# Performance work log

Measured on AMD Instinct MI355X. Metric: run time of the kernel, lower is better.

The kernel has to match this reference:

```python
import jax, jax.numpy as jnp
import numpy as np

N = 100000
E = 1600000
EMB = 64
IN = 64
HID = 64
HEADS = 3
NEG_SLOPE = 0.2            # PyG GATConv default LeakyReLU slope
RRELU_SLOPE = (1.0 / 8.0 + 1.0 / 3.0) / 2.0  # torch.rrelu eval-mode slope


def setup_inputs() -> dict:
    key = jax.random.key(0)
    ks = jax.random.split(key, 16)
    d_in = IN + EMB
    inp = {
        "z": jax.random.normal(ks[0], (N, EMB), jnp.float32),
        "x": jax.random.normal(ks[1], (N, IN), jnp.float32),
        "edge_index": jax.random.randint(ks[2], (2, E), 0, N, jnp.int32),
        # gat1: (in+emb) -> hidden, 3 heads, concat=False
        "W1": jax.random.normal(ks[3], (d_in, HEADS * HID), jnp.float32) / np.sqrt(d_in),
        "att_src1": jax.random.normal(ks[4], (HEADS, HID), jnp.float32) / np.sqrt(HID),
        "att_dst1": jax.random.normal(ks[5], (HEADS, HID), jnp.float32) / np.sqrt(HID),
        "bias1": jnp.zeros((HID,), jnp.float32),
        # gat2: hidden -> hidden, 3 heads, concat=True
        "W2": jax.random.normal(ks[6], (HID, HEADS * HID), jnp.float32) / np.sqrt(HID),
        "att_src2": jax.random.normal(ks[7], (HEADS, HID), jnp.float32) / np.sqrt(HID),
        "att_dst2": jax.random.normal(ks[8], (HEADS, HID), jnp.float32) / np.sqrt(HID),
        "bias2": jnp.zeros((HEADS * HID,), jnp.float32),
        # final linear hidden*3 -> 1 (with bias)
        "lin_w": jax.random.normal(ks[9], (HEADS * HID, 1), jnp.float32) / np.sqrt(HEADS * HID),
        "lin_b": jnp.zeros((1,), jnp.float32),
    }
    return inp


def rrelu_eval(x):
    return jnp.where(x >= 0, x, x * RRELU_SLOPE)


def gat_conv(x, src, dst, W, a_src, a_dst, bias, concat):
    """PyG GATConv (shared src/dst projection, self-loops already appended)."""
    n = x.shape[0]
    H, C = a_src.shape
    xl = (x @ W).reshape(n, H, C)                       # [N, H, C]
    s = jnp.einsum('nhc,hc->nh', xl, a_src)             # alpha_src per node
    d = jnp.einsum('nhc,hc->nh', xl, a_dst)             # alpha_dst per node
    alpha = jax.nn.leaky_relu(s[src] + d[dst], NEG_SLOPE)  # [E', H]
    amax = jax.ops.segment_max(alpha, dst, num_segments=n)
    ex = jnp.exp(alpha - amax[dst])
    denom = jax.ops.segment_sum(ex, dst, num_segments=n)
    w = ex / (denom[dst] + 1e-16)                       # segment softmax
    out = jax.ops.segment_sum(xl[src] * w[:, :, None], dst, num_segments=n)  # [N,H,C]
    out = out.reshape(n, H * C) if concat else out.mean(axis=1)
    return out + bias


def reference(z, x, edge_index, W1, att_src1, att_dst1, bias1,
              W2, att_src2, att_dst2, bias2, lin_w, lin_b):
    n = x.shape[0]
    loops = jnp.arange(n, dtype=edge_index.dtype)
    src = jnp.concatenate([edge_index[0], loops])       # add self-loops (PyG default)
    dst = jnp.concatenate([edge_index[1], loops])
    h = jnp.concatenate([z, x], axis=1)
    h = rrelu_eval(gat_conv(h, src, dst, W1, att_src1, att_dst1, bias1, concat=False))
    h = rrelu_eval(gat_conv(h, src, dst, W2, att_src2, att_dst2, bias2, concat=True))
    return h @ lin_w + lin_b
```

## Files before the change

kernel.cpp:

```cpp
#include <hip/hip_runtime.h>
#include <cstdint>
#include <cstddef>

#define NEG_SLOPE 0.2f
#define RRELU_SLOPE 0.22916666666666666f

#define BSHIFT 6
#define BCAP 1536
#define MAXNB 1600

typedef _Float16 half4 __attribute__((ext_vector_type(4)));
typedef _Float16 half8 __attribute__((ext_vector_type(8)));
typedef float f32x4 __attribute__((ext_vector_type(4)));

__device__ __forceinline__ float wave_sum64(float v) {
#pragma unroll
  for (int o = 32; o > 0; o >>= 1) v += __shfl_xor(v, o, 64);
  return v;
}

__global__ __launch_bounds__(256) void wcvt_kernel(const float* __restrict__ W1,
                                                   const float* __restrict__ W2,
                                                   _Float16* __restrict__ Wt1,
                                                   _Float16* __restrict__ Wt2) {
  const int c = blockIdx.x;
  for (int k = threadIdx.x; k < 128; k += 256)
    Wt1[(size_t)c * 128 + k] = (_Float16)W1[(size_t)k * 192 + c];
  for (int k = threadIdx.x; k < 64; k += 256)
    Wt2[(size_t)c * 64 + k] = (_Float16)W2[(size_t)k * 192 + c];
}

__device__ __forceinline__ void bucketA_body(char* smem, int bid, int nblk,
                                             const int* __restrict__ src,
                                             const int* __restrict__ dst, int E, int NB,
                                             int* __restrict__ cursor,
                                             int* __restrict__ region) {
  int* hist = (int*)smem;
  int* gbase = hist + MAXNB;
  const int tid = threadIdx.x;
  const int chunk = (E + nblk - 1) / nblk;
  const int e0 = bid * chunk;
  const int e1 = min(e0 + chunk, E);
  for (int b = tid; b < NB; b += 256) hist[b] = 0;
  __syncthreads();
  for (int i = e0 + tid; i < e1; i += 256) {
    atomicAdd(&hist[dst[i] >> BSHIFT], 1);
  }
  __syncthreads();
  for (int b = tid; b < NB; b += 256) {
    int c = hist[b];
    gbase[b] = (c > 0) ? atomicAdd(&cursor[b], c) : 0;
    hist[b] = 0;
  }
  __syncthreads();
  for (int i = e0 + tid; i < e1; i += 256) {
    int d = dst[i];
    int b = d >> BSHIFT;
    int idx = atomicAdd(&hist[b], 1) + gbase[b];
    if (idx < BCAP) region[b * BCAP + idx] = src[i] | ((d & 63) << 17);
  }
}

__global__ __launch_bounds__(256) void bucket_scan(const int* __restrict__ cursor, int NB,
                                                   int* __restrict__ colbase) {
  __shared__ int lds[256];
  const int tid = threadIdx.x;
  const int K = (NB + 255) / 256;
  int vals[8];
  int s = 0;
#pragma unroll
  for (int j = 0; j < 8; j++) {
    int b = tid * K + j;
    int v = (j < K && b < NB) ? (min(cursor[b], BCAP) + 64) : 0;
    vals[j] = v;
    s += v;
  }
  lds[tid] = s;
  __syncthreads();
  for (int o = 1; o < 256; o <<= 1) {
    int t = (tid >= o) ? lds[tid - o] : 0;
    __syncthreads();
    lds[tid] += t;
    __syncthreads();
  }
  int off = (tid > 0) ? lds[tid - 1] : 0;
#pragma unroll
  for (int j = 0; j < 8; j++) {
    int b = tid * K + j;
    if (j < K && b < NB) colbase[b] = off;
    off += vals[j];
  }
}

__global__ __launch_bounds__(256) void bucketB(const int* __restrict__ region,
                                               const int* __restrict__ cursor,
                                               const int* __restrict__ colbase, int NB,
                                               int* __restrict__ rp, int* __restrict__ col) {
  __shared__ int lcnt[64];
  __shared__ int loff[64];
  const int b = blockIdx.x;
  const int tid = threadIdx.x;
  const int cnt = min(cursor[b], BCAP);
  const int base = colbase[b];
  if (tid < 64) lcnt[tid] = 0;
  __syncthreads();
  const int* reg = region + (size_t)b * BCAP;
  for (int i = tid; i < cnt; i += 256) {
    atomicAdd(&lcnt[reg[i] >> 17], 1);
  }
  __syncthreads();
  if (tid < 64) {
    int v = lcnt[tid] + 1;
    int inc = v;
#pragma unroll
    for (int o = 1; o < 64; o <<= 1) {
      int t = __shfl_up(inc, o, 64);
      if (tid >= o) inc += t;
    }
    int excl = inc - v;
    loff[tid] = excl;
    int n = (b << BSHIFT) + tid;
    rp[n] = base + excl;
    col[base + excl] = n;
    lcnt[tid] = 1;
  }
  __syncthreads();
  for (int i = tid; i < cnt; i += 256) {
    int r = reg[i];
    int ld = r >> 17;
    int idx = atomicAdd(&lcnt[ld], 1);
    col[base + loff[ld] + idx] = r & 0x1FFFF;
  }
}

#define APAD 72
#define BTPAD 72
#define GEMM_LDS (64 * APAD * 2 + 192 * BTPAD * 2)

template <int KC>
__device__ __forceinline__ void gemm_body(char* smem, int bid,
    const float* __restrict__ A0, const float* __restrict__ A1,
    const _Float16* __restrict__ Wt, const float* __restrict__ asrc,
    const float* __restrict__ adst, _Float16* __restrict__ xlh,
    float* __restrict__ sdS, float* __restrict__ sdD, int N) {
  _Float16* A16 = (_Float16*)smem;
  _Float16* Bt = A16 + 64 * APAD;
  const int tid = threadIdx.x;
  const int w = tid >> 6;
  const int lane = tid & 63;
  const int m = lane & 15;
  const int q = lane >> 4;
  const int m0 = bid * 64;
  const int KW = KC * 64;

  f32x4 acc[12];
#pragma unroll
  for (int t = 0; t < 12; t++) acc[t] = (f32x4)(0.f);

  for (int kc = 0; kc < KC; kc++) {
    const float* __restrict__ Ab = (KC == 2 && kc == 1) ? A1 : A0;
    if (kc > 0) __syncthreads();
#pragma unroll
    for (int i = 0; i < 4; i++) {
      int f = tid + 256 * i;
      int row = f >> 4;
      int c4 = f & 15;
      int gr = m0 + row;
      gr = (gr < N) ? gr : (N - 1);
      float4 v = *(const float4*)(Ab + (size_t)gr * 64 + c4 * 4);
      half4 hv;
      hv.x = (_Float16)v.x; hv.y = (_Float16)v.y;
      hv.z = (_Float16)v.z; hv.w = (_Float16)v.w;
      *(half4*)&A16[row * APAD + c4 * 4] = hv;
    }
#pragma unroll
    for (int i = 0; i < 6; i++) {
      int f = tid + 256 * i;
      int kg = f / 192;
      int c = f % 192;
      half8 hv = *(const half8*)&Wt[(size_t)c * KW + kc * 64 + kg * 8];
      *(half8*)&Bt[c * BTPAD + kg * 8] = hv;
    }
    __syncthreads();

#pragma unroll
    for (int t = 0; t < 2; t++) {
      half8 af = *(const half8*)&A16[(w * 16 + m) * APAD + t * 32 + q * 8];
#pragma unroll
      for (int ct = 0; ct < 12; ct++) {
        half8 bf = *(const half8*)&Bt[(ct * 16 + m) * BTPAD + t * 32 + q * 8];
        acc[ct] = __builtin_amdgcn_mfma_f32_16x16x32_f16(af, bf, acc[ct], 0, 0, 0);
      }
    }
  }

  float avs[12], avd[12];
#pragma unroll
  for (int ct = 0; ct < 12; ct++) {
    avs[ct] = asrc[ct * 16 + m];
    avd[ct] = adst[ct * 16 + m];
  }
#pragma unroll
  for (int r = 0; r < 4; r++) {
    const int gr = m0 + w * 16 + q * 4 + r;
    const bool ok = gr < N;
    if (ok) {
#pragma unroll
      for (int ct = 0; ct < 12; ct++) {
        xlh[(size_t)gr * 192 + ct * 16 + m] = (_Float16)acc[ct][r];
      }
    }
#pragma unroll
    for (int h = 0; h < 3; h++) {
      float ps = acc[h * 4 + 0][r] * avs[h * 4 + 0] + acc[h * 4 + 1][r] * avs[h * 4 + 1] +
                 acc[h * 4 + 2][r] * avs[h * 4 + 2] + acc[h * 4 + 3][r] * avs[h * 4 + 3];
      float pd = acc[h * 4 + 0][r] * avd[h * 4 + 0] + acc[h * 4 + 1][r] * avd[h * 4 + 1] +
                 acc[h * 4 + 2][r] * avd[h * 4 + 2] + acc[h * 4 + 3][r] * avd[h * 4 + 3];
#pragma unroll
      for (int o = 1; o < 16; o <<= 1) {
        ps += __shfl_xor(ps, o, 64);
        pd += __shfl_xor(pd, o, 64);
      }
      if (ok && m == 0) {
        sdS[(size_t)gr * 4 + h] = ps;
        sdD[(size_t)gr * 4 + h] = pd;
      }
    }
  }
}

template <int KC>
__global__ __launch_bounds__(256, 4) void gemm_bucketA_fused(
    const float* __restrict__ A0, const float* __restrict__ A1,
    const _Float16* __restrict__ Wt, const float* __restrict__ asrc,
    const float* __restrict__ adst, _Float16* __restrict__ xlh,
    float* __restrict__ sdS, float* __restrict__ sdD, int N,
    const int* __restrict__ src, const int* __restrict__ dst, int E, int NB,
    int* __restrict__ cursor, int* __restrict__ region, int NBA) {
  extern __shared__ char smem[];
  if ((int)blockIdx.x < NBA) {
    bucketA_body(smem, blockIdx.x, NBA, src, dst, E, NB, cursor, region);
  } else {
    gemm_body<KC>(smem, blockIdx.x - NBA, A0, A1, Wt, asrc, adst, xlh, sdS, sdD, N);
  }
}

template <int D>
__device__ __forceinline__ void gather_fma_d(const _Float16* __restrict__ xlh,
                                             const float4* __restrict__ eb, int t, int par,
                                             unsigned laneoff, int h, float* acc) {
  half8 xv[D];
#pragma unroll
  for (int u = 0; u < D; u++) {
    float4 rec = eb[2 * (t + u) + par];
    unsigned off = (unsigned)__float_as_int(rec.x) * 384u + laneoff;
    xv[u] = *(const half8*)((const char*)xlh + off);
  }
#pragma unroll
  for (int u = 0; u < D; u++) {
    float4 rec = eb[2 * (t + u) + par];
    float w = (h == 0) ? rec.y : ((h == 1) ? rec.z : rec.w);
#pragma unroll
    for (int k = 0; k < 8; k++) acc[k] += (float)xv[u][k] * w;
  }
}

template <int MODE>
__global__ __launch_bounds__(256) void agg_kernel(
    const _Float16* __restrict__ xlh, const float4* __restrict__ sdS,
    const float4* __restrict__ sdD, const int* __restrict__ rp,
    const int* __restrict__ col, const float* __restrict__ bias,
    const float* __restrict__ lw, const float* __restrict__ lb,
    float* __restrict__ out, int N) {
  __shared__ float4 ebuf[4][64];
  const int lane = threadIdx.x & 63;
  const int wv = threadIdx.x >> 6;
  const int n = blockIdx.x * 4 + wv;
  if (n >= N) return;
  const int beg = rp[n], end = rp[n + 1];
  const float4 dd = sdD[n];
  const int s = lane & 31;
  const int h = (s < 24) ? (s >> 3) : 0;
  const int g = s & 7;
  const int par = lane >> 5;
  const unsigned laneoff = (unsigned)(h * 128 + g * 16);

  float l0 = 0.f, l1 = 0.f, l2 = 0.f;
  float acc[8];
#pragma unroll
  for (int k = 0; k < 8; k++) acc[k] = 0.f;

  for (int j0 = beg; j0 < end; j0 += 64) {
    const int cntc = min(64, end - j0);
    const bool valid = lane < cntc;
    int srcv = valid ? col[j0 + lane] : 0;
    float4 s4 = sdS[srcv];
    float t0 = s4.x + dd.x, t1 = s4.y + dd.y, t2 = s4.z + dd.z;
    t0 = (t0 < 0.f) ? t0 * NEG_SLOPE : t0;
    t1 = (t1 < 0.f) ? t1 * NEG_SLOPE : t1;
    t2 = (t2 < 0.f) ? t2 * NEG_SLOPE : t2;
    float e0 = valid ? __expf(t0) : 0.f;
    float e1 = valid ? __expf(t1) : 0.f;
    float e2 = valid ? __expf(t2) : 0.f;
    l0 += e0; l1 += e1; l2 += e2;
    ebuf[wv][lane] = make_float4(__int_as_float(srcv), e0, e1, e2);
    const float4* eb = ebuf[wv];
    const int steps = (cntc + 1) >> 1;
    int t = 0;
    for (; t + 7 <= steps; t += 7) {
      gather_fma_d<7>(xlh, eb, t, par, laneoff, h, acc);
    }
    if (t + 4 <= steps) {
      gather_fma_d<4>(xlh, eb, t, par, laneoff, h, acc);
      t += 4;
    }
    if (t + 2 <= steps) {
      gather_fma_d<2>(xlh, eb, t, par, laneoff, h, acc);
      t += 2;
    }
    if (t < steps) {
      gather_fma_d<1>(xlh, eb, t, par, laneoff, h, acc);
    }
  }

#pragma unroll
  for (int k = 0; k < 8; k++) acc[k] += __shfl_xor(acc[k], 32, 64);
  l0 = wave_sum64(l0);
  l1 = wave_sum64(l1);
  l2 = wave_sum64(l2);
  const float invl = 1.0f / (((h == 0) ? l0 : ((h == 1) ? l1 : l2)) + 1e-16f);
  float v[8];
#pragma unroll
  for (int k = 0; k < 8; k++) v[k] = acc[k] * invl;

  if (MODE == 1) {
    float m[8];
#pragma unroll
    for (int k = 0; k < 8; k++) {
      float a0 = __shfl(v[k], g, 64);
      float a1 = __shfl(v[k], g + 8, 64);
      float a2 = __shfl(v[k], g + 16, 64);
      m[k] = (a0 + a1 + a2) * (1.f / 3.f);
    }
    if (lane < 8) {
      float4 b0 = *(const float4*)(bias + g * 8);
      float4 b1 = *(const float4*)(bias + g * 8 + 4);
      float4 r0, r1;
      r0.x = m[0] + b0.x; r0.y = m[1] + b0.y; r0.z = m[2] + b0.z; r0.w = m[3] + b0.w;
      r1.x = m[4] + b1.x; r1.y = m[5] + b1.y; r1.z = m[6] + b1.z; r1.w = m[7] + b1.w;
      r0.x = (r0.x < 0.f) ? r0.x * RRELU_SLOPE : r0.x;
      r0.y = (r0.y < 0.f) ? r0.y * RRELU_SLOPE : r0.y;
      r0.z = (r0.z < 0.f) ? r0.z * RRELU_SLOPE : r0.z;
      r0.w = (r0.w < 0.f) ? r0.w * RRELU_SLOPE : r0.w;
      r1.x = (r1.x < 0.f) ? r1.x * RRELU_SLOPE : r1.x;
      r1.y = (r1.y < 0.f) ? r1.y * RRELU_SLOPE : r1.y;
      r1.z = (r1.z < 0.f) ? r1.z * RRELU_SLOPE : r1.z;
      r1.w = (r1.w < 0.f) ? r1.w * RRELU_SLOPE : r1.w;
      *(float4*)(out + (size_t)n * 64 + g * 8) = r0;
      *(float4*)(out + (size_t)n * 64 + g * 8 + 4) = r1;
    }
  } else {
    float part = 0.f;
    if (lane < 24) {
      const int c0 = h * 64 + g * 8;
      float4 b0 = *(const float4*)(bias + c0);
      float4 b1 = *(const float4*)(bias + c0 + 4);
      float4 w0 = *(const float4*)(lw + c0);
      float4 w1 = *(const float4*)(lw + c0 + 4);
      float r;
      r = v[0] + b0.x; r = (r < 0.f) ? r * RRELU_SLOPE : r; part += r * w0.x;
      r = v[1] + b0.y; r = (r < 0.f) ? r * RRELU_SLOPE : r; part += r * w0.y;
      r = v[2] + b0.z; r = (r < 0.f) ? r * RRELU_SLOPE : r; part += r * w0.z;
      r = v[3] + b0.w; r = (r < 0.f) ? r * RRELU_SLOPE : r; part += r * w0.w;
      r = v[4] + b1.x; r = (r < 0.f) ? r * RRELU_SLOPE : r; part += r * w1.x;
      r = v[5] + b1.y; r = (r < 0.f) ? r * RRELU_SLOPE : r; part += r * w1.y;
      r = v[6] + b1.z; r = (r < 0.f) ? r * RRELU_SLOPE : r; part += r * w1.z;
      r = v[7] + b1.w; r = (r < 0.f) ? r * RRELU_SLOPE : r; part += r * w1.w;
    }
    part = wave_sum64(part);
    if (lane == 0) out[n] = part + lb[0];
  }
}

extern "C" void kernel_launch(void* const* d_in, const int* in_sizes, int n_in,
                              void* d_out, int out_size, void* d_ws, size_t ws_size,
                              hipStream_t stream) {
  const float* z   = (const float*)d_in[0];
  const float* x   = (const float*)d_in[1];
  const int*   ei  = (const int*)d_in[2];
  const float* W1  = (const float*)d_in[3];
  const float* as1 = (const float*)d_in[4];
  const float* ad1 = (const float*)d_in[5];
  const float* b1  = (const float*)d_in[6];
  const float* W2  = (const float*)d_in[7];
  const float* as2 = (const float*)d_in[8];
  const float* ad2 = (const float*)d_in[9];
  const float* b2  = (const float*)d_in[10];
  const float* lw  = (const float*)d_in[11];
  const float* lb  = (const float*)d_in[12];
  float* out = (float*)d_out;

  const int N = in_sizes[0] / 64;
  const int E = in_sizes[2] / 2;
  const int* srcA = ei;
  const int* dstA = ei + E;
  const int NB = (N + 63) >> BSHIFT;
  const int NBA = 128;

  char* ws = (char*)d_ws;
  size_t off = 0;
  auto alloc = [&](size_t bytes) -> void* {
    void* p = ws + off;
    off = (off + bytes + 255) & ~(size_t)255;
    return p;
  };
  _Float16* xlh = (_Float16*)alloc((size_t)N * 192 * 2);
  float* h1  = (float*)alloc((size_t)N * 64 * 4);
  float* sdS = (float*)alloc((size_t)N * 4 * 4);
  float* sdD = (float*)alloc((size_t)N * 4 * 4);
  _Float16* Wt1 = (_Float16*)alloc((size_t)192 * 128 * 2);
  _Float16* Wt2 = (_Float16*)alloc((size_t)192 * 64 * 2);
  int* region  = (int*)alloc((size_t)NB * BCAP * 4);
  int* cursor  = (int*)alloc((size_t)NB * 4);
  int* colbase = (int*)alloc((size_t)NB * 4);
  int* rp      = (int*)alloc(((size_t)NB * 64 + 1) * 4);
  int* col     = (int*)alloc(((size_t)E + (size_t)NB * 64) * 4);
  if (off > ws_size) return;

  hipMemsetAsync(cursor, 0, (size_t)NB * 4, stream);
  wcvt_kernel<<<192, 256, 0, stream>>>(W1, W2, Wt1, Wt2);

  const int gg = (N + 63) / 64;
  gemm_bucketA_fused<2><<<NBA + gg, 256, GEMM_LDS, stream>>>(
      z, x, Wt1, as1, ad1, xlh, sdS, sdD, N, srcA, dstA, E, NB, cursor, region, NBA);
  bucket_scan<<<1, 256, 0, stream>>>(cursor, NB, colbase);
  bucketB<<<NB, 256, 0, stream>>>(region, cursor, colbase, NB, rp, col);

  agg_kernel<1><<<(N + 3) / 4, 256, 0, stream>>>(xlh, (const float4*)sdS, (const float4*)sdD,
                                                 rp, col, b1, nullptr, nullptr, h1, N);
  gemm_bucketA_fused<1><<<gg, 256, GEMM_LDS, stream>>>(
      h1, nullptr, Wt2, as2, ad2, xlh, sdS, sdD, N, nullptr, nullptr, 0, NB, nullptr, nullptr, 0);
  agg_kernel<2><<<(N + 3) / 4, 256, 0, stream>>>(xlh, (const float4*)sdS, (const float4*)sdD,
                                                 rp, col, b2, lw, lb, out, N);
}
```

Measured before the change: 417.9 us.

## Fuse layer-2 projection GEMM into layer-1 aggregation epilogue

The layer-1 aggregation kernel now computes the second layer's 64x192 projection per node right after the softmax-weighted sum. It reads W2 in fp16 through per-lane global loads and shuffle broadcasts, then writes xlh2 and the attention logits sdS2/sdD2 directly. This removes the separate GEMM launch and the fp32 h1 round trip through memory, but needs double-buffered xl/sd arrays and adds scalar FMA work and many cross-lane reductions per node.

```diff
diff --git a/kernel.cpp b/kernel.cpp
--- a/kernel.cpp
+++ b/kernel.cpp
@@ -271,7 +271,10 @@
     const float4* __restrict__ sdD, const int* __restrict__ rp,
     const int* __restrict__ col, const float* __restrict__ bias,
     const float* __restrict__ lw, const float* __restrict__ lb,
-    float* __restrict__ out, int N) {
+    float* __restrict__ out, int N,
+    const _Float16* __restrict__ w2t, const float* __restrict__ as2,
+    const float* __restrict__ ad2, _Float16* __restrict__ xlh2,
+    float* __restrict__ sdS2, float* __restrict__ sdD2) {
   __shared__ float4 ebuf[4][64];
   const int lane = threadIdx.x & 63;
   const int wv = threadIdx.x >> 6;
@@ -334,30 +337,57 @@
   for (int k = 0; k < 8; k++) v[k] = acc[k] * invl;
 
   if (MODE == 1) {
-    float m[8];
+    float hv_[8];
 #pragma unroll
     for (int k = 0; k < 8; k++) {
       float a0 = __shfl(v[k], g, 64);
       float a1 = __shfl(v[k], g + 8, 64);
       float a2 = __shfl(v[k], g + 16, 64);
-      m[k] = (a0 + a1 + a2) * (1.f / 3.f);
-    }
-    if (lane < 8) {
+      hv_[k] = (a0 + a1 + a2) * (1.f / 3.f);
+    }
+    {
       float4 b0 = *(const float4*)(bias + g * 8);
       float4 b1 = *(const float4*)(bias + g * 8 + 4);
-      float4 r0, r1;
-      r0.x = m[0] + b0.x; r0.y = m[1] + b0.y; r0.z = m[2] + b0.z; r0.w = m[3] + b0.w;
-      r1.x = m[4] + b1.x; r1.y = m[5] + b1.y; r1.z = m[6] + b1.z; r1.w = m[7] + b1.w;
-      r0.x = (r0.x < 0.f) ? r0.x * RRELU_SLOPE : r0.x;
-      r0.y = (r0.y < 0.f) ? r0.y * RRELU_SLOPE : r0.y;
-      r0.z = (r0.z < 0.f) ? r0.z * RRELU_SLOPE : r0.z;
-      r0.w = (r0.w < 0.f) ? r0.w * RRELU_SLOPE : r0.w;
-      r1.x = (r1.x < 0.f) ? r1.x * RRELU_SLOPE : r1.x;
-      r1.y = (r1.y < 0.f) ? r1.y * RRELU_SLOPE : r1.y;
-      r1.z = (r1.z < 0.f) ? r1.z * RRELU_SLOPE : r1.z;
-      r1.w = (r1.w < 0.f) ? r1.w * RRELU_SLOPE : r1.w;
-      *(float4*)(out + (size_t)n * 64 + g * 8) = r0;
-      *(float4*)(out + (size_t)n * 64 + g * 8 + 4) = r1;
+      hv_[0] += b0.x; hv_[1] += b0.y; hv_[2] += b0.z; hv_[3] += b0.w;
+      hv_[4] += b1.x; hv_[5] += b1.y; hv_[6] += b1.z; hv_[7] += b1.w;
+#pragma unroll
+      for (int k = 0; k < 8; k++) hv_[k] = (hv_[k] < 0.f) ? hv_[k] * RRELU_SLOPE : hv_[k];
+    }
+    float a20 = 0.f, a21 = 0.f, a22 = 0.f;
+    const half8* w0p = (const half8*)(w2t + (size_t)lane * 64);
+    const half8* w1p = (const half8*)(w2t + (size_t)(lane + 64) * 64);
+    const half8* w2p = (const half8*)(w2t + (size_t)(lane + 128) * 64);
+#pragma unroll
+    for (int kg = 0; kg < 8; kg++) {
+      float hb[8];
+#pragma unroll
+      for (int j = 0; j < 8; j++) hb[j] = __shfl(hv_[j], kg, 64);
+      half8 w0 = w0p[kg];
+      half8 w1 = w1p[kg];
+      half8 w2 = w2p[kg];
+#pragma unroll
+      for (int j = 0; j < 8; j++) {
+        a20 += hb[j] * (float)w0[j];
+        a21 += hb[j] * (float)w1[j];
+        a22 += hb[j] * (float)w2[j];
+      }
+    }
+    xlh2[(size_t)n * 192 + lane] = (_Float16)a20;
+    xlh2[(size_t)n * 192 + 64 + lane] = (_Float16)a21;
+    xlh2[(size_t)n * 192 + 128 + lane] = (_Float16)a22;
+    float ps0 = wave_sum64(a20 * as2[lane]);
+    float ps1 = wave_sum64(a21 * as2[64 + lane]);
+    float ps2 = wave_sum64(a22 * as2[128 + lane]);
+    float pd0 = wave_sum64(a20 * ad2[lane]);
+    float pd1 = wave_sum64(a21 * ad2[64 + lane]);
+    float pd2 = wave_sum64(a22 * ad2[128 + lane]);
+    if (lane == 0) {
+      sdS2[(size_t)n * 4 + 0] = ps0;
+      sdS2[(size_t)n * 4 + 1] = ps1;
+      sdS2[(size_t)n * 4 + 2] = ps2;
+      sdD2[(size_t)n * 4 + 0] = pd0;
+      sdD2[(size_t)n * 4 + 1] = pd1;
+      sdD2[(size_t)n * 4 + 2] = pd2;
     }
   } else {
     float part = 0.f;
@@ -414,10 +444,12 @@
     off = (off + bytes + 255) & ~(size_t)255;
     return p;
   };
-  _Float16* xlh = (_Float16*)alloc((size_t)N * 192 * 2);
-  float* h1  = (float*)alloc((size_t)N * 64 * 4);
-  float* sdS = (float*)alloc((size_t)N * 4 * 4);
-  float* sdD = (float*)alloc((size_t)N * 4 * 4);
+  _Float16* xlh  = (_Float16*)alloc((size_t)N * 192 * 2);
+  _Float16* xlh2 = (_Float16*)alloc((size_t)N * 192 * 2);
+  float* sdS  = (float*)alloc((size_t)N * 4 * 4);
+  float* sdD  = (float*)alloc((size_t)N * 4 * 4);
+  float* sdS2 = (float*)alloc((size_t)N * 4 * 4);
+  float* sdD2 = (float*)alloc((size_t)N * 4 * 4);
   _Float16* Wt1 = (_Float16*)alloc((size_t)192 * 128 * 2);
   _Float16* Wt2 = (_Float16*)alloc((size_t)192 * 64 * 2);
   int* region  = (int*)alloc((size_t)NB * BCAP * 4);
@@ -436,10 +468,10 @@
   bucket_scan<<<1, 256, 0, stream>>>(cursor, NB, colbase);
   bucketB<<<NB, 256, 0, stream>>>(region, cursor, colbase, NB, rp, col);
 
-  agg_kernel<1><<<(N + 3) / 4, 256, 0, stream>>>(xlh, (const float4*)sdS, (const float4*)sdD,
-                                                 rp, col, b1, nullptr, nullptr, h1, N);
-  gemm_bucketA_fused<1><<<gg, 256, GEMM_LDS, stream>>>(
-      h1, nullptr, Wt2, as2, ad2, xlh, sdS, sdD, N, nullptr, nullptr, 0, NB, nullptr, nullptr, 0);
-  agg_kernel<2><<<(N + 3) / 4, 256, 0, stream>>>(xlh, (const float4*)sdS, (const float4*)sdD,
-                                                 rp, col, b2, lw, lb, out, N);
-}
+  agg_kernel<1><<<(N + 3) / 4, 256, 0, stream>>>(
+      xlh, (const float4*)sdS, (const float4*)sdD, rp, col, b1, nullptr, nullptr,
+      nullptr, N, Wt2, as2, ad2, xlh2, sdS2, sdD2);
+  agg_kernel<2><<<(N + 3) / 4, 256, 0, stream>>>(
+      xlh2, (const float4*)sdS2, (const float4*)sdD2, rp, col, b2, lw, lb,
+      out, N, nullptr, nullptr, nullptr, nullptr, nullptr, nullptr);
+}
```

New measurement: 674.3 us. 1.61x slower.
